# Kernel optimization log

Measured on AMD Instinct MI355X. Metric: run time of the kernel, lower is better.

The kernel has to match this reference:

```python
import jax, jax.numpy as jnp
import numpy as np

DIM = 64  # per-head dim, matches init kwarg `dim`
SCALE = 1.0 / np.sqrt(DIM).astype(np.float32)


def setup_inputs() -> dict:
    key = jax.random.key(0)
    k1, k2, k3 = jax.random.split(key, 3)
    shape = (4, 16, 2048, DIM)  # [B, H, S, d]
    return {
        "q": jax.random.normal(k1, shape, dtype=jnp.float32),
        "k": jax.random.normal(k2, shape, dtype=jnp.float32),
        "v": jax.random.normal(k3, shape, dtype=jnp.float32),
    }


def reference(q, k, v):
    # attn = softmax(q @ k^T * scale) @ v  (dropout p=0.0 -> identity)
    scores = jnp.einsum("bhqd,bhkd->bhqk", q, k) * SCALE  # [B,H,S,S]
    attn = jax.nn.softmax(scores, axis=-1)
    return jnp.einsum("bhqk,bhkd->bhqd", attn, v)
```

## Files before the change

### kernel.cpp

```cpp
#include <hip/hip_runtime.h>
#include <hip/hip_bf16.h>

typedef __attribute__((ext_vector_type(8))) short bf16x8;
typedef __attribute__((ext_vector_type(16))) float f32x16;
typedef __attribute__((ext_vector_type(4))) float f32x4;
typedef __attribute__((ext_vector_type(2))) float f32x2;
typedef __attribute__((ext_vector_type(4))) unsigned short us4;
typedef __attribute__((ext_vector_type(8))) unsigned short us8;
typedef __attribute__((ext_vector_type(4))) unsigned int u32x4;

#define SEQ   2048
#define HDIM  64
#define QBLK  256
#define KVBLK 64
#define NT    (SEQ / KVBLK)
#define NBH   64

#if __has_builtin(__builtin_amdgcn_exp2f)
#define EXP2(x) __builtin_amdgcn_exp2f(x)
#else
#define EXP2(x) exp2f(x)
#endif
#define QSCALE 0.18033688011112042f

typedef const __attribute__((address_space(1))) unsigned int* gptr_t;
typedef __attribute__((address_space(3))) unsigned int* lptr_t;

__device__ inline unsigned short f2bf(float f) {
    return __builtin_bit_cast(unsigned short, __float2bfloat16(f));
}
__device__ inline unsigned pack_rz(float a, float b) {
    const unsigned ua = __builtin_bit_cast(unsigned, a) + 0x8000u;
    const unsigned ub = __builtin_bit_cast(unsigned, b) + 0x8000u;
    return (ua >> 16) | (ub & 0xFFFF0000u);
}

#define VCH 128
__global__ __launch_bounds__(256) void prep_kv(const float* __restrict__ K,
                                               const float* __restrict__ V,
                                               unsigned short* __restrict__ Kb,
                                               unsigned short* __restrict__ VT) {
    __shared__ unsigned short T[HDIM][VCH + 4];
    const int t   = threadIdx.x;
    const int bh  = blockIdx.y;
    const int kv0 = blockIdx.x * VCH;

    {
        const float* Ks = K + (size_t)bh * SEQ * HDIM + (size_t)kv0 * HDIM;
        unsigned short* Ko = Kb + (size_t)bh * SEQ * HDIM + (size_t)kv0 * HDIM;
        #pragma unroll
        for (int i = 0; i < 4; ++i) {
            const size_t e = ((size_t)(i * 256 + t)) * 8;
            const f32x4 a = *(const f32x4*)(Ks + e);
            const f32x4 b = *(const f32x4*)(Ks + e + 4);
            us8 h;
            #pragma unroll
            for (int j = 0; j < 4; ++j) { h[j] = f2bf(a[j]); h[4 + j] = f2bf(b[j]); }
            *(us8*)(Ko + e) = h;
        }
    }

    const float* Vb = V + (size_t)bh * SEQ * HDIM + (size_t)kv0 * HDIM;
    #pragma unroll
    for (int i = 0; i < 8; ++i) {
        const int idx = i * 256 + t;
        const int kv  = idx >> 4;
        const int d4  = idx & 15;
        const f32x4 v = *(const f32x4*)(Vb + (size_t)kv * HDIM + d4 * 4);
        #pragma unroll
        for (int j = 0; j < 4; ++j) T[d4 * 4 + j][kv] = f2bf(v[j]);
    }
    __syncthreads();
    unsigned short* Ob = VT + (size_t)bh * SEQ * HDIM + kv0;
    #pragma unroll
    for (int i = 0; i < 8; ++i) {
        const int o    = i * 256 + t;
        const int d    = o >> 5;
        const int slot = o & 31;
        const us4 h = *(const us4*)(&T[d][slot * 4]);
        *(us4*)(Ob + (size_t)d * SEQ + slot * 4) = h;
    }
}

__global__ __launch_bounds__(512, 4) void attn_fwd(
    const float* __restrict__ Q, const unsigned short* __restrict__ Kb,
    const unsigned short* __restrict__ VTb, float* __restrict__ O)
{
    __shared__ unsigned short K_lds[3][KVBLK * HDIM];
    __shared__ unsigned short VT_lds[3][HDIM * KVBLK];

    const int tid  = threadIdx.x;
    const int lane = tid & 63;
    const int wid  = tid >> 6;
    const int l31  = lane & 31;
    const int hi   = lane >> 5;

    const int qtile = blockIdx.x;
    const int bh    = blockIdx.y;

    const float*          Qb  = Q   + (size_t)bh * SEQ * HDIM;
    const unsigned short* Kbh = Kb  + (size_t)bh * SEQ * HDIM;
    const unsigned short* Vbh = VTb + (size_t)bh * SEQ * HDIM;
    float*                Ob  = O   + (size_t)bh * SEQ * HDIM;

    const int lr = lane >> 3;
    const int lx = ((lane & 7) ^ lr) << 4;

    bf16x8 qfrag[4];
    {
        const float* qp = Qb + (size_t)(qtile*QBLK + wid*32 + l31)*HDIM + 8*hi;
        #pragma unroll
        for (int kc = 0; kc < 4; ++kc) {
            const f32x4 a = *(const f32x4*)(qp + 16*kc);
            const f32x4 b = *(const f32x4*)(qp + 16*kc + 4);
            bf16x8 f;
            #pragma unroll
            for (int j = 0; j < 4; ++j) {
                f[j]   = (short)f2bf(a[j] * QSCALE);
                f[4+j] = (short)f2bf(b[j] * QSCALE);
            }
            qfrag[kc] = f;
        }
    }

    f32x16 acc0 = {}, acc1 = {};
    float l_run = 0.f;

    #define STAGE(T_, B_) do {                                                 \
        const char* Ks_ = (const char*)Kbh + (size_t)(T_) * 8192;              \
        const char* Vs_ = (const char*)Vbh + (size_t)(T_) * 128;               \
        const int row_ = wid * 8 + lr;                                         \
        __builtin_amdgcn_global_load_lds(                                      \
            (gptr_t)(Ks_ + row_ * 128 + lx),                                   \
            (lptr_t)((char*)K_lds[B_] + wid * 1024), 16, 0, 0);                \
        __builtin_amdgcn_global_load_lds(                                      \
            (gptr_t)(Vs_ + (size_t)row_ * (SEQ * 2) + lx),                     \
            (lptr_t)((char*)VT_lds[B_] + wid * 1024), 16, 0, 0);               \
    } while (0)

    STAGE(0, 0);
    STAGE(1, 1);
    asm volatile("s_waitcnt vmcnt(2)" ::: "memory");
    __builtin_amdgcn_s_barrier();

    int b = 0;
    for (int t = 0; t < NT; ++t) {
        if (t + 2 < NT) {
            int b2 = b + 2; if (b2 >= 3) b2 -= 3;
            STAGE(t + 2, b2);
        }

        const char* Kc = (const char*)K_lds[b];
        const char* Vc = (const char*)VT_lds[b];

        f32x16 s0 = {}, s1 = {};
        __builtin_amdgcn_s_setprio(1);
        #pragma unroll
        for (int kc = 0; kc < 4; ++kc) {
            const int sw = (l31 & 7) << 4;
            const bf16x8 kf0 = *(const bf16x8*)(Kc + l31*128        + (((2*kc+hi) << 4) ^ sw));
            s0 = __builtin_amdgcn_mfma_f32_32x32x16_bf16(kf0, qfrag[kc], s0, 0, 0, 0);
            const bf16x8 kf1 = *(const bf16x8*)(Kc + (32+l31)*128   + (((2*kc+hi) << 4) ^ sw));
            s1 = __builtin_amdgcn_mfma_f32_32x32x16_bf16(kf1, qfrag[kc], s1, 0, 0, 0);
        }
        __builtin_amdgcn_s_setprio(0);

        f32x2 ts2 = {0.f, 0.f};
        unsigned W0[8], W1[8];
        #pragma unroll
        for (int m = 0; m < 8; ++m) {
            const f32x2 p0 = { EXP2(s0[2*m]), EXP2(s0[2*m+1]) };
            const f32x2 p1 = { EXP2(s1[2*m]), EXP2(s1[2*m+1]) };
            ts2 += p0 + p1;
            W0[m] = pack_rz(p0[0], p0[1]);
            W1[m] = pack_rz(p1[0], p1[1]);
        }
        l_run += ts2[0] + ts2[1];

        __builtin_amdgcn_s_setprio(1);
        #pragma unroll
        for (int c = 0; c < 4; ++c) {
            unsigned pw[4];
            #pragma unroll
            for (int p = 0; p < 2; ++p) {
                const int i0 = 4*(c&1) + p;
                const int i1 = i0 + 2;
                const unsigned w_lo = (c >> 1) ? W1[i0] : W0[i0];
                const unsigned w_hi = (c >> 1) ? W1[i1] : W0[i1];
                const unsigned keep = hi ? w_hi : w_lo;
                const unsigned expo = hi ? w_lo : w_hi;
                const unsigned swp  = (unsigned)__shfl_xor((int)expo, 32, 64);
                pw[p]     = hi ? swp  : keep;
                pw[2 + p] = hi ? keep : swp;
            }
            const bf16x8 pf = __builtin_bit_cast(bf16x8, (u32x4){pw[0], pw[1], pw[2], pw[3]});
            const int sw0 = (l31 & 7) << 4;
            const bf16x8 vf0 = *(const bf16x8*)(Vc + l31*128      + (((2*c+hi) << 4) ^ sw0));
            acc0 = __builtin_amdgcn_mfma_f32_32x32x16_bf16(vf0, pf, acc0, 0, 0, 0);
            const bf16x8 vf1 = *(const bf16x8*)(Vc + (32+l31)*128 + (((2*c+hi) << 4) ^ sw0));
            acc1 = __builtin_amdgcn_mfma_f32_32x32x16_bf16(vf1, pf, acc1, 0, 0, 0);
        }
        __builtin_amdgcn_s_setprio(0);

        if (t + 2 < NT) {
            asm volatile("s_waitcnt vmcnt(2)" ::: "memory");
            __builtin_amdgcn_s_barrier();
        } else if (t + 1 < NT) {
            asm volatile("s_waitcnt vmcnt(0)" ::: "memory");
            __builtin_amdgcn_s_barrier();
        }
        if (++b == 3) b = 0;
    }

    const float l_tot = l_run + __shfl_xor(l_run, 32, 64);
    const float inv = 1.0f / l_tot;
    float* op = Ob + (size_t)(qtile*QBLK + wid*32 + l31)*HDIM + 4*hi;
    #pragma unroll
    for (int g = 0; g < 4; ++g) {
        f32x4 o;
        o[0] = acc0[4*g]   * inv; o[1] = acc0[4*g+1] * inv;
        o[2] = acc0[4*g+2] * inv; o[3] = acc0[4*g+3] * inv;
        *(f32x4*)(op + 8*g) = o;
        f32x4 o2;
        o2[0] = acc1[4*g]   * inv; o2[1] = acc1[4*g+1] * inv;
        o2[2] = acc1[4*g+2] * inv; o2[3] = acc1[4*g+3] * inv;
        *(f32x4*)(op + 32 + 8*g) = o2;
    }
    #undef STAGE
}

extern "C" void kernel_launch(void* const* d_in, const int* in_sizes, int n_in,
                              void* d_out, int out_size, void* d_ws, size_t ws_size,
                              hipStream_t stream) {
    const float* q = (const float*)d_in[0];
    const float* k = (const float*)d_in[1];
    const float* v = (const float*)d_in[2];
    float* o = (float*)d_out;

    unsigned short* Kb = (unsigned short*)d_ws;
    unsigned short* VT = (unsigned short*)((char*)d_ws + (size_t)NBH*SEQ*HDIM*2);

    prep_kv<<<dim3(SEQ / VCH, NBH), dim3(256), 0, stream>>>(k, v, Kb, VT);

    dim3 grid(SEQ / QBLK, NBH);
    attn_fwd<<<grid, dim3(512), 0, stream>>>(q, Kb, VT, o);
}
```

Baseline: 113.8 us.

## Double-buffer KV tile pairs and remap blocks so each head stays on one XCD

The three-buffer rolling prefetch (one barrier per KV tile) becomes four LDS buffers used as two ping-pong pairs. Each iteration prefetches two tiles, computes two, then waits and barriers once. The 2D grid is also flattened to 1D and remapped so all q-tiles of a head land on the same XCD, improving L2 reuse of K/V. In exchange LDS per block grows from 48KB to 64KB, which may limit occupancy, and the full vmcnt(0) wait can expose load latency.

```diff
diff --git a/kernel.cpp b/kernel.cpp
--- a/kernel.cpp
+++ b/kernel.cpp
@@ -86,8 +86,8 @@
     const float* __restrict__ Q, const unsigned short* __restrict__ Kb,
     const unsigned short* __restrict__ VTb, float* __restrict__ O)
 {
-    __shared__ unsigned short K_lds[3][KVBLK * HDIM];
-    __shared__ unsigned short VT_lds[3][HDIM * KVBLK];
+    __shared__ unsigned short K_lds[4][KVBLK * HDIM];
+    __shared__ unsigned short VT_lds[4][HDIM * KVBLK];
 
     const int tid  = threadIdx.x;
     const int lane = tid & 63;
@@ -95,8 +95,11 @@
     const int l31  = lane & 31;
     const int hi   = lane >> 5;
 
-    const int qtile = blockIdx.x;
-    const int bh    = blockIdx.y;
+    const int id    = blockIdx.x;
+    const int xcd   = id & 7;
+    const int slot  = id >> 3;
+    const int qtile = slot & 7;
+    const int bh    = xcd * 8 + (slot >> 3);
 
     const float*          Qb  = Q   + (size_t)bh * SEQ * HDIM;
     const unsigned short* Kbh = Kb  + (size_t)bh * SEQ * HDIM;
@@ -132,35 +135,24 @@
         const int row_ = wid * 8 + lr;                                         \
         __builtin_amdgcn_global_load_lds(                                      \
             (gptr_t)(Ks_ + row_ * 128 + lx),                                   \
-            (lptr_t)((char*)K_lds[B_] + wid * 1024), 16, 0, 0);                \
+            (lptr_t)((char*)K_lds + (B_) * 8192 + wid * 1024), 16, 0, 0);      \
         __builtin_amdgcn_global_load_lds(                                      \
             (gptr_t)(Vs_ + (size_t)row_ * (SEQ * 2) + lx),                     \
-            (lptr_t)((char*)VT_lds[B_] + wid * 1024), 16, 0, 0);               \
+            (lptr_t)((char*)VT_lds + (B_) * 8192 + wid * 1024), 16, 0, 0);     \
     } while (0)
 
-    STAGE(0, 0);
-    STAGE(1, 1);
-    asm volatile("s_waitcnt vmcnt(2)" ::: "memory");
-    __builtin_amdgcn_s_barrier();
-
-    int b = 0;
-    for (int t = 0; t < NT; ++t) {
-        if (t + 2 < NT) {
-            int b2 = b + 2; if (b2 >= 3) b2 -= 3;
-            STAGE(t + 2, b2);
-        }
-
-        const char* Kc = (const char*)K_lds[b];
-        const char* Vc = (const char*)VT_lds[b];
+    auto compute_tile = [&](int buf) {
+        const char* Kc = (const char*)K_lds + buf * 8192;
+        const char* Vc = (const char*)VT_lds + buf * 8192;
+        const int sw = (l31 & 7) << 4;
 
         f32x16 s0 = {}, s1 = {};
         __builtin_amdgcn_s_setprio(1);
         #pragma unroll
         for (int kc = 0; kc < 4; ++kc) {
-            const int sw = (l31 & 7) << 4;
-            const bf16x8 kf0 = *(const bf16x8*)(Kc + l31*128        + (((2*kc+hi) << 4) ^ sw));
+            const bf16x8 kf0 = *(const bf16x8*)(Kc + l31*128      + (((2*kc+hi) << 4) ^ sw));
             s0 = __builtin_amdgcn_mfma_f32_32x32x16_bf16(kf0, qfrag[kc], s0, 0, 0, 0);
-            const bf16x8 kf1 = *(const bf16x8*)(Kc + (32+l31)*128   + (((2*kc+hi) << 4) ^ sw));
+            const bf16x8 kf1 = *(const bf16x8*)(Kc + (32+l31)*128 + (((2*kc+hi) << 4) ^ sw));
             s1 = __builtin_amdgcn_mfma_f32_32x32x16_bf16(kf1, qfrag[kc], s1, 0, 0, 0);
         }
         __builtin_amdgcn_s_setprio(0);
@@ -194,22 +186,32 @@
                 pw[2 + p] = hi ? keep : swp;
             }
             const bf16x8 pf = __builtin_bit_cast(bf16x8, (u32x4){pw[0], pw[1], pw[2], pw[3]});
-            const int sw0 = (l31 & 7) << 4;
-            const bf16x8 vf0 = *(const bf16x8*)(Vc + l31*128      + (((2*c+hi) << 4) ^ sw0));
+            const bf16x8 vf0 = *(const bf16x8*)(Vc + l31*128      + (((2*c+hi) << 4) ^ sw));
             acc0 = __builtin_amdgcn_mfma_f32_32x32x16_bf16(vf0, pf, acc0, 0, 0, 0);
-            const bf16x8 vf1 = *(const bf16x8*)(Vc + (32+l31)*128 + (((2*c+hi) << 4) ^ sw0));
+            const bf16x8 vf1 = *(const bf16x8*)(Vc + (32+l31)*128 + (((2*c+hi) << 4) ^ sw));
             acc1 = __builtin_amdgcn_mfma_f32_32x32x16_bf16(vf1, pf, acc1, 0, 0, 0);
         }
         __builtin_amdgcn_s_setprio(0);
-
-        if (t + 2 < NT) {
-            asm volatile("s_waitcnt vmcnt(2)" ::: "memory");
-            __builtin_amdgcn_s_barrier();
-        } else if (t + 1 < NT) {
+    };
+
+    STAGE(0, 0);
+    STAGE(1, 1);
+    asm volatile("s_waitcnt vmcnt(0)" ::: "memory");
+    __builtin_amdgcn_s_barrier();
+
+    for (int i = 0; i < NT / 2; ++i) {
+        const int tt = 2 * i;
+        const int pc = (i & 1) ? 2 : 0;
+        const int ps = 2 - pc;
+        if (tt + 2 < NT) { STAGE(tt + 2, ps); STAGE(tt + 3, ps + 1); }
+
+        compute_tile(pc);
+        compute_tile(pc + 1);
+
+        if (tt + 2 < NT) {
             asm volatile("s_waitcnt vmcnt(0)" ::: "memory");
             __builtin_amdgcn_s_barrier();
         }
-        if (++b == 3) b = 0;
     }
 
     const float l_tot = l_run + __shfl_xor(l_run, 32, 64);
@@ -242,6 +244,5 @@
 
     prep_kv<<<dim3(SEQ / VCH, NBH), dim3(256), 0, stream>>>(k, v, Kb, VT);
 
-    dim3 grid(SEQ / QBLK, NBH);
-    attn_fwd<<<grid, dim3(512), 0, stream>>>(q, Kb, VT, o);
-}
+    attn_fwd<<<dim3(512), dim3(512), 0, stream>>>(q, Kb, VT, o);
+}
```

Result: faster. 109.7 us, median of 2 (-3.5%).
